# Performance work log

Hardware: AMD Instinct MI355X
Metric: run time of the kernel (lower is better)

Reference implementation:

```python
import jax, jax.numpy as jnp
import numpy as np
from jax import lax

KERNEL = 5  # cv2 np.ones((5,5)) structuring element
EDGE_WEIGHT = 0.1


def _edge_weights(target):
    # target: [B,1,H,W] float. Binary mask -> morphological gradient via
    # max-pool (dilate) and min-pool (erode) with 5x5 window, SAME padding.
    # cv2 pads dilate with -inf and erode with +inf, so padding never
    # creates or removes foreground; reduce_window init values match that.
    b = (target > 0.5).astype(target.dtype)
    win = (1, 1, KERNEL, KERNEL)
    ones = (1, 1, 1, 1)
    dilated = lax.reduce_window(b, jnp.float32(-jnp.inf), lax.max, win, ones, 'SAME')
    eroded = lax.reduce_window(b, jnp.float32(jnp.inf), lax.min, win, ones, 'SAME')
    edge = dilated - eroded
    # Samples with empty masks get edge==0 everywhere, so the per-sample
    # binary_mask.sum()>0 guard in the original is a no-op here.
    return jnp.where(edge > 0, jnp.float32(EDGE_WEIGHT), jnp.float32(1.0))


def setup_inputs() -> dict:
    key = jax.random.key(0)
    k1, k2 = jax.random.split(key)
    shape = (32, 1, 1024, 1024)
    pred = jax.random.normal(k1, shape, dtype=jnp.float32)
    target = jax.random.randint(k2, shape, 0, 2).astype(jnp.float32)
    return {"pred": pred, "target": target}


def reference(pred, target):
    # BCEWithLogitsLoss(reduction='none'): softplus(x) - x*t (stable form)
    loss = jax.nn.softplus(pred) - pred * target
    # Weighting branch only taken when target.max()==1 and target.min()==0
    cond = jnp.logical_and(target.max() == 1.0, target.min() == 0.0)
    weights = _edge_weights(target)
    weights = jnp.where(cond, weights, jnp.float32(1.0))
    return (loss * weights).mean()
```

## Files before the change

kernel.cpp:

```cpp
#include <hip/hip_runtime.h>


#define IMG     1024
#define BAND    32
#define NBANDS  (IMG / BAND)
#define NIMG    32
#define WORDS   16
#define HALO    2
#define MAXROWS (BAND + 2 * HALO)
#define NTOT    33554432.0

typedef unsigned long long u64;

__device__ __forceinline__ unsigned encf(float f) {
    unsigned u = __float_as_uint(f);
    return (u & 0x80000000u) ? ~u : (u | 0x80000000u);
}
__device__ __forceinline__ float decf(unsigned e) {
    unsigned u = (e & 0x80000000u) ? (e & 0x7fffffffu) : ~e;
    return __uint_as_float(u);
}

__global__ void bbl_init(double* dws, unsigned* uws) {
    if (threadIdx.x == 0) {
        dws[0] = 0.0; dws[1] = 0.0;
        uws[0] = 0xFFFFFFFFu;
        uws[1] = 0u;
    }
}

__global__ __launch_bounds__(512) void bbl_main(
        const float* __restrict__ pred,
        const float* __restrict__ target,
        double* __restrict__ dws, unsigned* __restrict__ uws) {
    __shared__ u64 Bm[MAXROWS][WORDS];
    __shared__ u64 Vd[BAND][WORDS];
    __shared__ u64 Ve[BAND][WORDS];
    __shared__ u64 Em[BAND][WORDS];
    __shared__ float    redS1[8], redSe[8];
    __shared__ unsigned redMn[8], redMx[8];

    const int tid  = threadIdx.x;
    const int lane = tid & 63;
    const int wid  = tid >> 6;
    const int img  = blockIdx.x / NBANDS;
    const int r0   = (blockIdx.x % NBANDS) * BAND;
    const int hs   = max(r0 - HALO, 0);
    const int he   = min(r0 + BAND + HALO, IMG);
    const int nLoaded = he - hs;
    const size_t base = (size_t)img * IMG * IMG;

    float vmin = 3.4e38f, vmax = -3.4e38f;

    for (int lr = wid; lr < nLoaded; lr += 8) {
        const float4* rowp = (const float4*)(target + base + (size_t)(hs + lr) * IMG);
        #pragma unroll
        for (int it = 0; it < 4; ++it) {
            float4 v = rowp[it * 64 + lane];
            vmin = fminf(vmin, fminf(fminf(v.x, v.y), fminf(v.z, v.w)));
            vmax = fmaxf(vmax, fmaxf(fmaxf(v.x, v.y), fmaxf(v.z, v.w)));
            u64 b0 = __ballot(v.x > 0.5f);
            u64 b1 = __ballot(v.y > 0.5f);
            u64 b2 = __ballot(v.z > 0.5f);
            u64 b3 = __ballot(v.w > 0.5f);
            if (lane < 4) {
                u64 w = (lane == 0) ? b0 : (lane == 1) ? b1 : (lane == 2) ? b2 : b3;
                Bm[lr][it * 4 + lane] = w;
            }
        }
    }
    __syncthreads();

    {
        const int orow = tid >> 4, w = tid & 15;
        const int gr = r0 + orow;
        const int lo = max(gr - 2, 0), hi = min(gr + 2, IMG - 1);
        u64 vd = 0ULL, ve = ~0ULL;
        for (int g = lo; g <= hi; ++g) { u64 b = Bm[g - hs][w]; vd |= b; ve &= b; }
        Vd[orow][w] = vd; Ve[orow][w] = ve;
    }
    __syncthreads();

    {
        const int orow = tid >> 4, w = tid & 15;
        const int k = w & 3;
        u64 hd = Vd[orow][w], he_ = Ve[orow][w];
        #pragma unroll
        for (int dd = 0; dd < 4; ++dd) {
            const int delta = (dd < 2) ? dd - 2 : dd - 1;
            const int kp = k + delta;
            u64 td, te;
            if (kp >= 0 && kp <= 3) {
                td = Vd[orow][w + delta];
                te = Ve[orow][w + delta];
            } else if (kp > 3) {
                const int wi = w + delta - 4, wn = w + delta;
                u64 nd = (wn <= 15) ? Vd[orow][wn] : 0ULL;
                u64 ne = (wn <= 15) ? Ve[orow][wn] : ~0ULL;
                td = (Vd[orow][wi] >> 1) | (nd << 63);
                te = (Ve[orow][wi] >> 1) | (ne << 63);
            } else {
                const int wi = w + delta + 4, wn = w + delta;
                u64 nd = (wn >= 0) ? Vd[orow][wn] : 0ULL;
                u64 ne = (wn >= 0) ? Ve[orow][wn] : ~0ULL;
                td = (Vd[orow][wi] << 1) | (nd >> 63);
                te = (Ve[orow][wi] << 1) | (ne >> 63);
            }
            hd |= td; he_ &= te;
        }
        Em[orow][w] = hd & ~he_;
    }
    __syncthreads();

    float s1 = 0.f, se = 0.f;
    for (int orow = wid * 4; orow < wid * 4 + 4; ++orow) {
        const int gr = r0 + orow, lr = gr - hs;
        const float4* rowp = (const float4*)(pred + base + (size_t)gr * IMG);
        #pragma unroll
        for (int it = 0; it < 4; ++it) {
            float4 p = rowp[it * 64 + lane];
            u64 e0 = Em[orow][it * 4 + 0], e1 = Em[orow][it * 4 + 1];
            u64 e2 = Em[orow][it * 4 + 2], e3 = Em[orow][it * 4 + 3];
            u64 t0 = Bm[lr][it * 4 + 0],   t1 = Bm[lr][it * 4 + 1];
            u64 t2 = Bm[lr][it * 4 + 2],   t3 = Bm[lr][it * 4 + 3];
            float x, t, loss;
            x = p.x; t = (float)((unsigned)((t0 >> lane) & 1ULL));
            loss = fmaxf(x, 0.f) - x * t + __logf(1.f + __expf(-fabsf(x)));
            s1 += loss; se += ((e0 >> lane) & 1ULL) ? loss : 0.f;
            x = p.y; t = (float)((unsigned)((t1 >> lane) & 1ULL));
            loss = fmaxf(x, 0.f) - x * t + __logf(1.f + __expf(-fabsf(x)));
            s1 += loss; se += ((e1 >> lane) & 1ULL) ? loss : 0.f;
            x = p.z; t = (float)((unsigned)((t2 >> lane) & 1ULL));
            loss = fmaxf(x, 0.f) - x * t + __logf(1.f + __expf(-fabsf(x)));
            s1 += loss; se += ((e2 >> lane) & 1ULL) ? loss : 0.f;
            x = p.w; t = (float)((unsigned)((t3 >> lane) & 1ULL));
            loss = fmaxf(x, 0.f) - x * t + __logf(1.f + __expf(-fabsf(x)));
            s1 += loss; se += ((e3 >> lane) & 1ULL) ? loss : 0.f;
        }
    }

    for (int off = 32; off > 0; off >>= 1) {
        s1   += __shfl_down(s1, off);
        se   += __shfl_down(se, off);
        vmin  = fminf(vmin, __shfl_down(vmin, off));
        vmax  = fmaxf(vmax, __shfl_down(vmax, off));
    }
    if (lane == 0) {
        redS1[wid] = s1; redSe[wid] = se;
        redMn[wid] = encf(vmin); redMx[wid] = encf(vmax);
    }
    __syncthreads();
    if (tid == 0) {
        float S1 = 0.f, Se = 0.f; unsigned mn = 0xFFFFFFFFu, mx = 0u;
        #pragma unroll
        for (int i = 0; i < 8; ++i) {
            S1 += redS1[i]; Se += redSe[i];
            mn = min(mn, redMn[i]); mx = max(mx, redMx[i]);
        }
        atomicAdd(&dws[0], (double)S1);
        atomicAdd(&dws[1], (double)Se);
        atomicMin(&uws[0], mn);
        atomicMax(&uws[1], mx);
    }
}

__global__ void bbl_fin(const double* __restrict__ dws,
                        const unsigned* __restrict__ uws,
                        float* __restrict__ out) {
    if (threadIdx.x == 0) {
        float fmin = decf(uws[0]);
        float fmax = decf(uws[1]);
        bool cond = (fmax == 1.0f) && (fmin == 0.0f);
        double s = cond ? (dws[0] - 0.9 * dws[1]) : dws[0];
        out[0] = (float)(s / NTOT);
    }
}

extern "C" void kernel_launch(void* const* d_in, const int* in_sizes, int n_in,
                              void* d_out, int out_size, void* d_ws, size_t ws_size,
                              hipStream_t stream) {
    const float* pred   = (const float*)d_in[0];
    const float* target = (const float*)d_in[1];
    double*   dws = (double*)d_ws;
    unsigned* uws = (unsigned*)(dws + 2);
    float*    out = (float*)d_out;

    hipLaunchKernelGGL(bbl_init, dim3(1), dim3(64), 0, stream, dws, uws);
    hipLaunchKernelGGL(bbl_main, dim3(NIMG * NBANDS), dim3(512), 0, stream,
                       pred, target, dws, uws);
    hipLaunchKernelGGL(bbl_fin, dim3(1), dim3(64), 0, stream, dws, uws, out);
}
```

Before: 296.3 us.

## Split target bit-packing into separate pass to avoid halo re-reads

Adds a first kernel that reads the target once, packs it into per-row 64-bit masks in workspace and computes min/max. A second kernel loads only the packed bits, including halo rows, plus pred to compute the loss. This removes the halo re-reads of the float target and lightens the main kernel. In exchange it adds a global write and read of the packed mask, an extra launch and a serialization point between the kernels. It also pads shared arrays and issues the pred loads up front. The old fused kernel is kept as a fallback when the workspace is too small.

```diff
diff --git a/kernel.cpp b/kernel.cpp
--- a/kernel.cpp
+++ b/kernel.cpp
@@ -6,8 +6,10 @@
 #define NBANDS  (IMG / BAND)
 #define NIMG    32
 #define WORDS   16
+#define WPAD    17
 #define HALO    2
 #define MAXROWS (BAND + 2 * HALO)
+#define NROWS   (NIMG * IMG)
 #define NTOT    33554432.0
 
 typedef unsigned long long u64;
@@ -29,16 +31,74 @@
     }
 }
 
-__global__ __launch_bounds__(512) void bbl_main(
+__global__ __launch_bounds__(256) void bbl_bits(
+        const float* __restrict__ target,
+        u64* __restrict__ bits, unsigned* __restrict__ uws) {
+    __shared__ unsigned redMn[4], redMx[4];
+    const int tid  = threadIdx.x;
+    const int lane = tid & 63;
+    const int wv   = tid >> 6;
+    const int waveId = blockIdx.x * 4 + wv;
+    const int nWaves = gridDim.x * 4;
+
+    float vmin = 3.4e38f, vmax = -3.4e38f;
+
+    for (int row = waveId; row < NROWS; row += nWaves) {
+        const float4* rowp = (const float4*)(target + (size_t)row * IMG);
+        float4 v0 = rowp[lane];
+        float4 v1 = rowp[64 + lane];
+        float4 v2 = rowp[128 + lane];
+        float4 v3 = rowp[192 + lane];
+
+        vmin = fminf(vmin, fminf(fminf(v0.x, v0.y), fminf(v0.z, v0.w)));
+        vmax = fmaxf(vmax, fmaxf(fmaxf(v0.x, v0.y), fmaxf(v0.z, v0.w)));
+        vmin = fminf(vmin, fminf(fminf(v1.x, v1.y), fminf(v1.z, v1.w)));
+        vmax = fmaxf(vmax, fmaxf(fmaxf(v1.x, v1.y), fmaxf(v1.z, v1.w)));
+        vmin = fminf(vmin, fminf(fminf(v2.x, v2.y), fminf(v2.z, v2.w)));
+        vmax = fmaxf(vmax, fmaxf(fmaxf(v2.x, v2.y), fmaxf(v2.z, v2.w)));
+        vmin = fminf(vmin, fminf(fminf(v3.x, v3.y), fminf(v3.z, v3.w)));
+        vmax = fmaxf(vmax, fmaxf(fmaxf(v3.x, v3.y), fmaxf(v3.z, v3.w)));
+
+        u64 myw = 0ULL;
+        #pragma unroll
+        for (int it = 0; it < 4; ++it) {
+            float4 v = (it == 0) ? v0 : (it == 1) ? v1 : (it == 2) ? v2 : v3;
+            u64 b0 = __ballot(v.x > 0.5f);
+            u64 b1 = __ballot(v.y > 0.5f);
+            u64 b2 = __ballot(v.z > 0.5f);
+            u64 b3 = __ballot(v.w > 0.5f);
+            if ((lane >> 2) == it) {
+                const int m = lane & 3;
+                myw = (m == 0) ? b0 : (m == 1) ? b1 : (m == 2) ? b2 : b3;
+            }
+        }
+        if (lane < 16) bits[(size_t)row * WORDS + lane] = myw;
+    }
+
+    for (int off = 32; off > 0; off >>= 1) {
+        vmin = fminf(vmin, __shfl_down(vmin, off));
+        vmax = fmaxf(vmax, __shfl_down(vmax, off));
+    }
+    if (lane == 0) { redMn[wv] = encf(vmin); redMx[wv] = encf(vmax); }
+    __syncthreads();
+    if (tid == 0) {
+        unsigned mn = 0xFFFFFFFFu, mx = 0u;
+        #pragma unroll
+        for (int i = 0; i < 4; ++i) { mn = min(mn, redMn[i]); mx = max(mx, redMx[i]); }
+        atomicMin(&uws[0], mn);
+        atomicMax(&uws[1], mx);
+    }
+}
+
+__global__ __launch_bounds__(512) void bbl_loss(
         const float* __restrict__ pred,
-        const float* __restrict__ target,
-        double* __restrict__ dws, unsigned* __restrict__ uws) {
-    __shared__ u64 Bm[MAXROWS][WORDS];
-    __shared__ u64 Vd[BAND][WORDS];
-    __shared__ u64 Ve[BAND][WORDS];
-    __shared__ u64 Em[BAND][WORDS];
-    __shared__ float    redS1[8], redSe[8];
-    __shared__ unsigned redMn[8], redMx[8];
+        const u64* __restrict__ bits,
+        double* __restrict__ dws) {
+    __shared__ u64 Bm[MAXROWS][WPAD];
+    __shared__ u64 Vd[BAND][WPAD];
+    __shared__ u64 Ve[BAND][WPAD];
+    __shared__ u64 Em[BAND][WPAD];
+    __shared__ float redS1[8], redSe[8];
 
     const int tid  = threadIdx.x;
     const int lane = tid & 63;
@@ -50,24 +110,10 @@
     const int nLoaded = he - hs;
     const size_t base = (size_t)img * IMG * IMG;
 
-    float vmin = 3.4e38f, vmax = -3.4e38f;
-
-    for (int lr = wid; lr < nLoaded; lr += 8) {
-        const float4* rowp = (const float4*)(target + base + (size_t)(hs + lr) * IMG);
-        #pragma unroll
-        for (int it = 0; it < 4; ++it) {
-            float4 v = rowp[it * 64 + lane];
-            vmin = fminf(vmin, fminf(fminf(v.x, v.y), fminf(v.z, v.w)));
-            vmax = fmaxf(vmax, fmaxf(fmaxf(v.x, v.y), fmaxf(v.z, v.w)));
-            u64 b0 = __ballot(v.x > 0.5f);
-            u64 b1 = __ballot(v.y > 0.5f);
-            u64 b2 = __ballot(v.z > 0.5f);
-            u64 b3 = __ballot(v.w > 0.5f);
-            if (lane < 4) {
-                u64 w = (lane == 0) ? b0 : (lane == 1) ? b1 : (lane == 2) ? b2 : b3;
-                Bm[lr][it * 4 + lane] = w;
-            }
-        }
+    {
+        const u64* gb = bits + ((size_t)img * IMG + hs) * WORDS;
+        for (int i = tid; i < nLoaded * WORDS; i += 512)
+            Bm[i >> 4][i & 15] = gb[i];
     }
     __syncthreads();
 
@@ -116,6 +162,137 @@
     for (int orow = wid * 4; orow < wid * 4 + 4; ++orow) {
         const int gr = r0 + orow, lr = gr - hs;
         const float4* rowp = (const float4*)(pred + base + (size_t)gr * IMG);
+        float4 p0 = rowp[lane];
+        float4 p1 = rowp[64 + lane];
+        float4 p2 = rowp[128 + lane];
+        float4 p3 = rowp[192 + lane];
+        #pragma unroll
+        for (int it = 0; it < 4; ++it) {
+            float4 p = (it == 0) ? p0 : (it == 1) ? p1 : (it == 2) ? p2 : p3;
+            u64 e0 = Em[orow][it * 4 + 0], e1 = Em[orow][it * 4 + 1];
+            u64 e2 = Em[orow][it * 4 + 2], e3 = Em[orow][it * 4 + 3];
+            u64 t0 = Bm[lr][it * 4 + 0],   t1 = Bm[lr][it * 4 + 1];
+            u64 t2 = Bm[lr][it * 4 + 2],   t3 = Bm[lr][it * 4 + 3];
+            float x, l;
+            x = p.x;
+            l = fmaxf(x, 0.f) + __logf(1.f + __expf(-fabsf(x)))
+                - (((t0 >> lane) & 1ULL) ? x : 0.f);
+            s1 += l; se += ((e0 >> lane) & 1ULL) ? l : 0.f;
+            x = p.y;
+            l = fmaxf(x, 0.f) + __logf(1.f + __expf(-fabsf(x)))
+                - (((t1 >> lane) & 1ULL) ? x : 0.f);
+            s1 += l; se += ((e1 >> lane) & 1ULL) ? l : 0.f;
+            x = p.z;
+            l = fmaxf(x, 0.f) + __logf(1.f + __expf(-fabsf(x)))
+                - (((t2 >> lane) & 1ULL) ? x : 0.f);
+            s1 += l; se += ((e2 >> lane) & 1ULL) ? l : 0.f;
+            x = p.w;
+            l = fmaxf(x, 0.f) + __logf(1.f + __expf(-fabsf(x)))
+                - (((t3 >> lane) & 1ULL) ? x : 0.f);
+            s1 += l; se += ((e3 >> lane) & 1ULL) ? l : 0.f;
+        }
+    }
+
+    for (int off = 32; off > 0; off >>= 1) {
+        s1 += __shfl_down(s1, off);
+        se += __shfl_down(se, off);
+    }
+    if (lane == 0) { redS1[wid] = s1; redSe[wid] = se; }
+    __syncthreads();
+    if (tid == 0) {
+        float S1 = 0.f, Se = 0.f;
+        #pragma unroll
+        for (int i = 0; i < 8; ++i) { S1 += redS1[i]; Se += redSe[i]; }
+        atomicAdd(&dws[0], (double)S1);
+        atomicAdd(&dws[1], (double)Se);
+    }
+}
+
+__global__ __launch_bounds__(512) void bbl_main(
+        const float* __restrict__ pred,
+        const float* __restrict__ target,
+        double* __restrict__ dws, unsigned* __restrict__ uws) {
+    __shared__ u64 Bm[MAXROWS][WORDS];
+    __shared__ u64 Vd[BAND][WORDS];
+    __shared__ u64 Ve[BAND][WORDS];
+    __shared__ u64 Em[BAND][WORDS];
+    __shared__ float    redS1[8], redSe[8];
+    __shared__ unsigned redMn[8], redMx[8];
+
+    const int tid  = threadIdx.x;
+    const int lane = tid & 63;
+    const int wid  = tid >> 6;
+    const int img  = blockIdx.x / NBANDS;
+    const int r0   = (blockIdx.x % NBANDS) * BAND;
+    const int hs   = max(r0 - HALO, 0);
+    const int he   = min(r0 + BAND + HALO, IMG);
+    const int nLoaded = he - hs;
+    const size_t base = (size_t)img * IMG * IMG;
+
+    float vmin = 3.4e38f, vmax = -3.4e38f;
+
+    for (int lr = wid; lr < nLoaded; lr += 8) {
+        const float4* rowp = (const float4*)(target + base + (size_t)(hs + lr) * IMG);
+        #pragma unroll
+        for (int it = 0; it < 4; ++it) {
+            float4 v = rowp[it * 64 + lane];
+            vmin = fminf(vmin, fminf(fminf(v.x, v.y), fminf(v.z, v.w)));
+            vmax = fmaxf(vmax, fmaxf(fmaxf(v.x, v.y), fmaxf(v.z, v.w)));
+            u64 b0 = __ballot(v.x > 0.5f);
+            u64 b1 = __ballot(v.y > 0.5f);
+            u64 b2 = __ballot(v.z > 0.5f);
+            u64 b3 = __ballot(v.w > 0.5f);
+            if (lane < 4) {
+                u64 w = (lane == 0) ? b0 : (lane == 1) ? b1 : (lane == 2) ? b2 : b3;
+                Bm[lr][it * 4 + lane] = w;
+            }
+        }
+    }
+    __syncthreads();
+    {
+        const int orow = tid >> 4, w = tid & 15;
+        const int gr = r0 + orow;
+        const int lo = max(gr - 2, 0), hi = min(gr + 2, IMG - 1);
+        u64 vd = 0ULL, ve = ~0ULL;
+        for (int g = lo; g <= hi; ++g) { u64 b = Bm[g - hs][w]; vd |= b; ve &= b; }
+        Vd[orow][w] = vd; Ve[orow][w] = ve;
+    }
+    __syncthreads();
+    {
+        const int orow = tid >> 4, w = tid & 15;
+        const int k = w & 3;
+        u64 hd = Vd[orow][w], he_ = Ve[orow][w];
+        #pragma unroll
+        for (int dd = 0; dd < 4; ++dd) {
+            const int delta = (dd < 2) ? dd - 2 : dd - 1;
+            const int kp = k + delta;
+            u64 td, te;
+            if (kp >= 0 && kp <= 3) {
+                td = Vd[orow][w + delta];
+                te = Ve[orow][w + delta];
+            } else if (kp > 3) {
+                const int wi = w + delta - 4, wn = w + delta;
+                u64 nd = (wn <= 15) ? Vd[orow][wn] : 0ULL;
+                u64 ne = (wn <= 15) ? Ve[orow][wn] : ~0ULL;
+                td = (Vd[orow][wi] >> 1) | (nd << 63);
+                te = (Ve[orow][wi] >> 1) | (ne << 63);
+            } else {
+                const int wi = w + delta + 4, wn = w + delta;
+                u64 nd = (wn >= 0) ? Vd[orow][wn] : 0ULL;
+                u64 ne = (wn >= 0) ? Ve[orow][wn] : ~0ULL;
+                td = (Vd[orow][wi] << 1) | (nd >> 63);
+                te = (Ve[orow][wi] << 1) | (ne >> 63);
+            }
+            hd |= td; he_ &= te;
+        }
+        Em[orow][w] = hd & ~he_;
+    }
+    __syncthreads();
+
+    float s1 = 0.f, se = 0.f;
+    for (int orow = wid * 4; orow < wid * 4 + 4; ++orow) {
+        const int gr = r0 + orow, lr = gr - hs;
+        const float4* rowp = (const float4*)(pred + base + (size_t)gr * IMG);
         #pragma unroll
         for (int it = 0; it < 4; ++it) {
             float4 p = rowp[it * 64 + lane];
@@ -185,8 +362,19 @@
     unsigned* uws = (unsigned*)(dws + 2);
     float*    out = (float*)d_out;
 
+    const size_t bits_off   = 64;
+    const size_t bits_bytes = (size_t)NROWS * WORDS * sizeof(u64);
+
     hipLaunchKernelGGL(bbl_init, dim3(1), dim3(64), 0, stream, dws, uws);
-    hipLaunchKernelGGL(bbl_main, dim3(NIMG * NBANDS), dim3(512), 0, stream,
-                       pred, target, dws, uws);
+    if (ws_size >= bits_off + bits_bytes) {
+        u64* bits = (u64*)((char*)d_ws + bits_off);
+        hipLaunchKernelGGL(bbl_bits, dim3(2048), dim3(256), 0, stream,
+                           target, bits, uws);
+        hipLaunchKernelGGL(bbl_loss, dim3(NIMG * NBANDS), dim3(512), 0, stream,
+                           pred, bits, dws);
+    } else {
+        hipLaunchKernelGGL(bbl_main, dim3(NIMG * NBANDS), dim3(512), 0, stream,
+                           pred, target, dws, uws);
+    }
     hipLaunchKernelGGL(bbl_fin, dim3(1), dim3(64), 0, stream, dws, uws, out);
 }
```

After: 308.1 us. +4.0%, slower.

## Split fused kernel into bit-pack, edge, and loss passes via workspace planes

Applied to the files above, without the earlier changes.

Replaces the single banded kernel with three kernels: one packs the target into a global bitmask plane while also reducing min/max, one computes the 5x5 morphological edge plane using wave shuffles instead of shared memory, and one streams pred with the bit planes to accumulate the loss sums. The aim is to drop the redundant halo reads of target and the shared-memory syncs, and to give each pass a simple grid-stride streaming pattern with two loads in flight. In exchange it adds two extra launches and the write and read of 8 MB of bit planes, and it falls back to the old kernel when the workspace is too small.

```diff
diff --git a/kernel.cpp b/kernel.cpp
--- a/kernel.cpp
+++ b/kernel.cpp
@@ -8,6 +8,9 @@
 #define WORDS   16
 #define HALO    2
 #define MAXROWS (BAND + 2 * HALO)
+#define NROWS   (NIMG * IMG)
+#define NGRP    (NROWS * 4)
+#define NWAVES  8192
 #define NTOT    33554432.0
 
 typedef unsigned long long u64;
@@ -26,6 +29,177 @@
         dws[0] = 0.0; dws[1] = 0.0;
         uws[0] = 0xFFFFFFFFu;
         uws[1] = 0u;
+    }
+}
+
+__global__ __launch_bounds__(256) void bbl_bits(
+        const float* __restrict__ target,
+        u64* __restrict__ bits, unsigned* __restrict__ uws) {
+    __shared__ unsigned redMn[4], redMx[4];
+    const int tid  = threadIdx.x;
+    const int lane = tid & 63;
+    const int wv   = tid >> 6;
+    const int waveId = __builtin_amdgcn_readfirstlane(blockIdx.x * 4 + wv);
+
+    float vmin = 3.4e38f, vmax = -3.4e38f;
+    const float4* tp = (const float4*)target;
+
+    for (int g = waveId; g < NGRP; g += 2 * NWAVES) {
+        const int g2 = g + NWAVES;
+        float4 a = tp[(size_t)g  * 64 + lane];
+        float4 b = tp[(size_t)g2 * 64 + lane];
+
+        vmin = fminf(vmin, fminf(fminf(a.x, a.y), fminf(a.z, a.w)));
+        vmax = fmaxf(vmax, fmaxf(fmaxf(a.x, a.y), fmaxf(a.z, a.w)));
+        vmin = fminf(vmin, fminf(fminf(b.x, b.y), fminf(b.z, b.w)));
+        vmax = fmaxf(vmax, fmaxf(fmaxf(b.x, b.y), fmaxf(b.z, b.w)));
+
+        u64 a0 = __ballot(a.x > 0.5f), a1 = __ballot(a.y > 0.5f);
+        u64 a2 = __ballot(a.z > 0.5f), a3 = __ballot(a.w > 0.5f);
+        u64 b0 = __ballot(b.x > 0.5f), b1 = __ballot(b.y > 0.5f);
+        u64 b2 = __ballot(b.z > 0.5f), b3 = __ballot(b.w > 0.5f);
+
+        const int m = lane & 3;
+        u64 wa = (m == 0) ? a0 : (m == 1) ? a1 : (m == 2) ? a2 : a3;
+        u64 wb = (m == 0) ? b0 : (m == 1) ? b1 : (m == 2) ? b2 : b3;
+        if (lane < 8) {
+            const int gg = (lane < 4) ? g : g2;
+            bits[(size_t)gg * 4 + m] = (lane < 4) ? wa : wb;
+        }
+    }
+
+    for (int off = 32; off > 0; off >>= 1) {
+        vmin = fminf(vmin, __shfl_down(vmin, off));
+        vmax = fmaxf(vmax, __shfl_down(vmax, off));
+    }
+    if (lane == 0) { redMn[wv] = encf(vmin); redMx[wv] = encf(vmax); }
+    __syncthreads();
+    if (tid == 0) {
+        unsigned mn = 0xFFFFFFFFu, mx = 0u;
+        #pragma unroll
+        for (int i = 0; i < 4; ++i) { mn = min(mn, redMn[i]); mx = max(mx, redMx[i]); }
+        atomicMin(&uws[0], mn);
+        atomicMax(&uws[1], mx);
+    }
+}
+
+__global__ __launch_bounds__(256) void bbl_edge(
+        const u64* __restrict__ bits, u64* __restrict__ eplane) {
+    const int tid  = threadIdx.x;
+    const int lane = tid & 63;
+    const int wv   = tid >> 6;
+    const int waveId = __builtin_amdgcn_readfirstlane(blockIdx.x * 4 + wv);
+
+    const int R  = waveId * 4 + (lane >> 4);
+    const int r  = R & (IMG - 1);
+    const int rb = R - r;
+    const int w  = lane & 15;
+
+    const int lo = max(r - 2, 0), hi = min(r + 2, IMG - 1);
+    u64 vd = 0ULL, ve = ~0ULL;
+    for (int rr = lo; rr <= hi; ++rr) {
+        u64 b = bits[(size_t)(rb + rr) * WORDS + w];
+        vd |= b; ve &= b;
+    }
+
+    const int k = w & 3;
+    u64 hd = vd, he_ = ve;
+    #pragma unroll
+    for (int dd = 0; dd < 4; ++dd) {
+        const int delta = (dd < 2) ? dd - 2 : dd - 1;
+        const int kp = k + delta;
+        u64 td, te;
+        if (kp >= 0 && kp <= 3) {
+            td = __shfl(vd, w + delta, 16);
+            te = __shfl(ve, w + delta, 16);
+        } else if (kp > 3) {
+            const int wi = w + delta - 4, wn = w + delta;
+            u64 vdi = __shfl(vd, wi, 16),      vei = __shfl(ve, wi, 16);
+            u64 vdn = __shfl(vd, wn & 15, 16), ven = __shfl(ve, wn & 15, 16);
+            u64 nd = (wn <= 15) ? vdn : 0ULL;
+            u64 ne = (wn <= 15) ? ven : ~0ULL;
+            td = (vdi >> 1) | (nd << 63);
+            te = (vei >> 1) | (ne << 63);
+        } else {
+            const int wi = w + delta + 4, wn = w + delta;
+            u64 vdi = __shfl(vd, wi, 16),      vei = __shfl(ve, wi, 16);
+            u64 vdn = __shfl(vd, wn & 15, 16), ven = __shfl(ve, wn & 15, 16);
+            u64 nd = (wn >= 0) ? vdn : 0ULL;
+            u64 ne = (wn >= 0) ? ven : ~0ULL;
+            td = (vdi << 1) | (nd >> 63);
+            te = (vei << 1) | (ne >> 63);
+        }
+        hd |= td; he_ &= te;
+    }
+    eplane[(size_t)R * WORDS + w] = hd & ~he_;
+}
+
+__global__ __launch_bounds__(256) void bbl_loss(
+        const float* __restrict__ pred,
+        const u64* __restrict__ bits, const u64* __restrict__ eplane,
+        double* __restrict__ dws) {
+    __shared__ float redS1[4], redSe[4];
+    const int tid  = threadIdx.x;
+    const int lane = tid & 63;
+    const int wv   = tid >> 6;
+    const int waveId = __builtin_amdgcn_readfirstlane(blockIdx.x * 4 + wv);
+
+    float s1 = 0.f, se = 0.f;
+    const float4* pp = (const float4*)pred;
+
+    for (int g = waveId; g < NGRP; g += 2 * NWAVES) {
+        const int g2 = g + NWAVES;
+        float4 a = pp[(size_t)g  * 64 + lane];
+        float4 b = pp[(size_t)g2 * 64 + lane];
+        u64 ta0 = bits[(size_t)g * 4 + 0],   ta1 = bits[(size_t)g * 4 + 1];
+        u64 ta2 = bits[(size_t)g * 4 + 2],   ta3 = bits[(size_t)g * 4 + 3];
+        u64 ea0 = eplane[(size_t)g * 4 + 0], ea1 = eplane[(size_t)g * 4 + 1];
+        u64 ea2 = eplane[(size_t)g * 4 + 2], ea3 = eplane[(size_t)g * 4 + 3];
+        u64 tb0 = bits[(size_t)g2 * 4 + 0],   tb1 = bits[(size_t)g2 * 4 + 1];
+        u64 tb2 = bits[(size_t)g2 * 4 + 2],   tb3 = bits[(size_t)g2 * 4 + 3];
+        u64 eb0 = eplane[(size_t)g2 * 4 + 0], eb1 = eplane[(size_t)g2 * 4 + 1];
+        u64 eb2 = eplane[(size_t)g2 * 4 + 2], eb3 = eplane[(size_t)g2 * 4 + 3];
+
+        float x, l;
+        x = a.x; l = fmaxf(x, 0.f) + __logf(1.f + __expf(-fabsf(x)))
+                    - (((ta0 >> lane) & 1ULL) ? x : 0.f);
+        s1 += l; se += ((ea0 >> lane) & 1ULL) ? l : 0.f;
+        x = a.y; l = fmaxf(x, 0.f) + __logf(1.f + __expf(-fabsf(x)))
+                    - (((ta1 >> lane) & 1ULL) ? x : 0.f);
+        s1 += l; se += ((ea1 >> lane) & 1ULL) ? l : 0.f;
+        x = a.z; l = fmaxf(x, 0.f) + __logf(1.f + __expf(-fabsf(x)))
+                    - (((ta2 >> lane) & 1ULL) ? x : 0.f);
+        s1 += l; se += ((ea2 >> lane) & 1ULL) ? l : 0.f;
+        x = a.w; l = fmaxf(x, 0.f) + __logf(1.f + __expf(-fabsf(x)))
+                    - (((ta3 >> lane) & 1ULL) ? x : 0.f);
+        s1 += l; se += ((ea3 >> lane) & 1ULL) ? l : 0.f;
+
+        x = b.x; l = fmaxf(x, 0.f) + __logf(1.f + __expf(-fabsf(x)))
+                    - (((tb0 >> lane) & 1ULL) ? x : 0.f);
+        s1 += l; se += ((eb0 >> lane) & 1ULL) ? l : 0.f;
+        x = b.y; l = fmaxf(x, 0.f) + __logf(1.f + __expf(-fabsf(x)))
+                    - (((tb1 >> lane) & 1ULL) ? x : 0.f);
+        s1 += l; se += ((eb1 >> lane) & 1ULL) ? l : 0.f;
+        x = b.z; l = fmaxf(x, 0.f) + __logf(1.f + __expf(-fabsf(x)))
+                    - (((tb2 >> lane) & 1ULL) ? x : 0.f);
+        s1 += l; se += ((eb2 >> lane) & 1ULL) ? l : 0.f;
+        x = b.w; l = fmaxf(x, 0.f) + __logf(1.f + __expf(-fabsf(x)))
+                    - (((tb3 >> lane) & 1ULL) ? x : 0.f);
+        s1 += l; se += ((eb3 >> lane) & 1ULL) ? l : 0.f;
+    }
+
+    for (int off = 32; off > 0; off >>= 1) {
+        s1 += __shfl_down(s1, off);
+        se += __shfl_down(se, off);
+    }
+    if (lane == 0) { redS1[wv] = s1; redSe[wv] = se; }
+    __syncthreads();
+    if (tid == 0) {
+        float S1 = 0.f, Se = 0.f;
+        #pragma unroll
+        for (int i = 0; i < 4; ++i) { S1 += redS1[i]; Se += redSe[i]; }
+        atomicAdd(&dws[0], (double)S1);
+        atomicAdd(&dws[1], (double)Se);
     }
 }
 
@@ -70,7 +244,6 @@
         }
     }
     __syncthreads();
-
     {
         const int orow = tid >> 4, w = tid & 15;
         const int gr = r0 + orow;
@@ -80,7 +253,6 @@
         Vd[orow][w] = vd; Ve[orow][w] = ve;
     }
     __syncthreads();
-
     {
         const int orow = tid >> 4, w = tid & 15;
         const int k = w & 3;
@@ -185,8 +357,23 @@
     unsigned* uws = (unsigned*)(dws + 2);
     float*    out = (float*)d_out;
 
+    const size_t bits_off  = 64;
+    const size_t plane_sz  = (size_t)NROWS * WORDS * sizeof(u64);
+    const size_t need      = bits_off + 2 * plane_sz;
+
     hipLaunchKernelGGL(bbl_init, dim3(1), dim3(64), 0, stream, dws, uws);
-    hipLaunchKernelGGL(bbl_main, dim3(NIMG * NBANDS), dim3(512), 0, stream,
-                       pred, target, dws, uws);
+    if (ws_size >= need) {
+        u64* bits   = (u64*)((char*)d_ws + bits_off);
+        u64* eplane = bits + (size_t)NROWS * WORDS;
+        hipLaunchKernelGGL(bbl_bits, dim3(2048), dim3(256), 0, stream,
+                           target, bits, uws);
+        hipLaunchKernelGGL(bbl_edge, dim3(2048), dim3(256), 0, stream,
+                           bits, eplane);
+        hipLaunchKernelGGL(bbl_loss, dim3(2048), dim3(256), 0, stream,
+                           pred, bits, eplane, dws);
+    } else {
+        hipLaunchKernelGGL(bbl_main, dim3(NIMG * NBANDS), dim3(512), 0, stream,
+                           pred, target, dws, uws);
+    }
     hipLaunchKernelGGL(bbl_fin, dim3(1), dim3(64), 0, stream, dws, uws, out);
 }
```

Measured after the change: 356.4 us. 1.2x slower.

## Halve block size and have each thread load two rows ahead of use

Applied to the files above, without the earlier changes.

The block shrinks from 512 to 256 threads, and every stage is reworked so each wave or thread covers twice as many rows. In the load stage, the target rows lr and lr+4, and the pred row pairs, are all fetched into registers up front before any compute. The goal is more memory loads in flight per wave to hide global-memory latency in what looks like a latency-bound kernel. The cost is higher register pressure, which could lower occupancy, and fewer threads per block doing the shared-memory bit-mask stages.

```diff
diff --git a/kernel.cpp b/kernel.cpp
--- a/kernel.cpp
+++ b/kernel.cpp
@@ -29,7 +29,7 @@
     }
 }
 
-__global__ __launch_bounds__(512) void bbl_main(
+__global__ __launch_bounds__(256) void bbl_main(
         const float* __restrict__ pred,
         const float* __restrict__ target,
         double* __restrict__ dws, unsigned* __restrict__ uws) {
@@ -37,8 +37,8 @@
     __shared__ u64 Vd[BAND][WORDS];
     __shared__ u64 Ve[BAND][WORDS];
     __shared__ u64 Em[BAND][WORDS];
-    __shared__ float    redS1[8], redSe[8];
-    __shared__ unsigned redMn[8], redMx[8];
+    __shared__ float    redS1[4], redSe[4];
+    __shared__ unsigned redMn[4], redMx[4];
 
     const int tid  = threadIdx.x;
     const int lane = tid & 63;
@@ -49,80 +49,153 @@
     const int he   = min(r0 + BAND + HALO, IMG);
     const int nLoaded = he - hs;
     const size_t base = (size_t)img * IMG * IMG;
+    const float* tb = target + base;
 
     float vmin = 3.4e38f, vmax = -3.4e38f;
 
+    #pragma unroll 1
     for (int lr = wid; lr < nLoaded; lr += 8) {
-        const float4* rowp = (const float4*)(target + base + (size_t)(hs + lr) * IMG);
+        const int lrB = lr + 4;
+        const bool hb = (lrB < nLoaded);
+        const float* rA = tb + (size_t)(hs + lr) * IMG + 4 * lane;
+        float4 a0 = *(const float4*)(rA);
+        float4 a1 = *(const float4*)(rA + 256);
+        float4 a2 = *(const float4*)(rA + 512);
+        float4 a3 = *(const float4*)(rA + 768);
+        float4 d0, d1, d2, d3;
+        if (hb) {
+            const float* rB = tb + (size_t)(hs + lrB) * IMG + 4 * lane;
+            d0 = *(const float4*)(rB);
+            d1 = *(const float4*)(rB + 256);
+            d2 = *(const float4*)(rB + 512);
+            d3 = *(const float4*)(rB + 768);
+        }
         #pragma unroll
         for (int it = 0; it < 4; ++it) {
-            float4 v = rowp[it * 64 + lane];
+            float4 v = (it == 0) ? a0 : (it == 1) ? a1 : (it == 2) ? a2 : a3;
             vmin = fminf(vmin, fminf(fminf(v.x, v.y), fminf(v.z, v.w)));
             vmax = fmaxf(vmax, fmaxf(fmaxf(v.x, v.y), fmaxf(v.z, v.w)));
-            u64 b0 = __ballot(v.x > 0.5f);
-            u64 b1 = __ballot(v.y > 0.5f);
-            u64 b2 = __ballot(v.z > 0.5f);
-            u64 b3 = __ballot(v.w > 0.5f);
+            u64 c0 = __ballot(v.x > 0.5f);
+            u64 c1 = __ballot(v.y > 0.5f);
+            u64 c2 = __ballot(v.z > 0.5f);
+            u64 c3 = __ballot(v.w > 0.5f);
             if (lane < 4) {
-                u64 w = (lane == 0) ? b0 : (lane == 1) ? b1 : (lane == 2) ? b2 : b3;
+                u64 w = (lane == 0) ? c0 : (lane == 1) ? c1 : (lane == 2) ? c2 : c3;
                 Bm[lr][it * 4 + lane] = w;
             }
         }
+        if (hb) {
+            #pragma unroll
+            for (int it = 0; it < 4; ++it) {
+                float4 v = (it == 0) ? d0 : (it == 1) ? d1 : (it == 2) ? d2 : d3;
+                vmin = fminf(vmin, fminf(fminf(v.x, v.y), fminf(v.z, v.w)));
+                vmax = fmaxf(vmax, fmaxf(fmaxf(v.x, v.y), fmaxf(v.z, v.w)));
+                u64 c0 = __ballot(v.x > 0.5f);
+                u64 c1 = __ballot(v.y > 0.5f);
+                u64 c2 = __ballot(v.z > 0.5f);
+                u64 c3 = __ballot(v.w > 0.5f);
+                if (lane < 4) {
+                    u64 w = (lane == 0) ? c0 : (lane == 1) ? c1 : (lane == 2) ? c2 : c3;
+                    Bm[lrB][it * 4 + lane] = w;
+                }
+            }
+        }
     }
     __syncthreads();
 
     {
-        const int orow = tid >> 4, w = tid & 15;
-        const int gr = r0 + orow;
-        const int lo = max(gr - 2, 0), hi = min(gr + 2, IMG - 1);
-        u64 vd = 0ULL, ve = ~0ULL;
-        for (int g = lo; g <= hi; ++g) { u64 b = Bm[g - hs][w]; vd |= b; ve &= b; }
-        Vd[orow][w] = vd; Ve[orow][w] = ve;
+        const int w = tid & 15;
+        #pragma unroll
+        for (int half = 0; half < 2; ++half) {
+            const int orow = (tid >> 4) + half * 16;
+            const int gr = r0 + orow;
+            const int lo = max(gr - 2, 0), hi = min(gr + 2, IMG - 1);
+            u64 vd = 0ULL, ve = ~0ULL;
+            for (int g = lo; g <= hi; ++g) { u64 bb = Bm[g - hs][w]; vd |= bb; ve &= bb; }
+            Vd[orow][w] = vd; Ve[orow][w] = ve;
+        }
     }
     __syncthreads();
 
     {
-        const int orow = tid >> 4, w = tid & 15;
+        const int w = tid & 15;
         const int k = w & 3;
-        u64 hd = Vd[orow][w], he_ = Ve[orow][w];
-        #pragma unroll
-        for (int dd = 0; dd < 4; ++dd) {
-            const int delta = (dd < 2) ? dd - 2 : dd - 1;
-            const int kp = k + delta;
-            u64 td, te;
-            if (kp >= 0 && kp <= 3) {
-                td = Vd[orow][w + delta];
-                te = Ve[orow][w + delta];
-            } else if (kp > 3) {
-                const int wi = w + delta - 4, wn = w + delta;
-                u64 nd = (wn <= 15) ? Vd[orow][wn] : 0ULL;
-                u64 ne = (wn <= 15) ? Ve[orow][wn] : ~0ULL;
-                td = (Vd[orow][wi] >> 1) | (nd << 63);
-                te = (Ve[orow][wi] >> 1) | (ne << 63);
-            } else {
-                const int wi = w + delta + 4, wn = w + delta;
-                u64 nd = (wn >= 0) ? Vd[orow][wn] : 0ULL;
-                u64 ne = (wn >= 0) ? Ve[orow][wn] : ~0ULL;
-                td = (Vd[orow][wi] << 1) | (nd >> 63);
-                te = (Ve[orow][wi] << 1) | (ne >> 63);
+        #pragma unroll
+        for (int half = 0; half < 2; ++half) {
+            const int orow = (tid >> 4) + half * 16;
+            u64 hd = Vd[orow][w], he_ = Ve[orow][w];
+            #pragma unroll
+            for (int dd = 0; dd < 4; ++dd) {
+                const int delta = (dd < 2) ? dd - 2 : dd - 1;
+                const int kp = k + delta;
+                u64 td, te;
+                if (kp >= 0 && kp <= 3) {
+                    td = Vd[orow][w + delta];
+                    te = Ve[orow][w + delta];
+                } else if (kp > 3) {
+                    const int wi = w + delta - 4, wn = w + delta;
+                    u64 nd = (wn <= 15) ? Vd[orow][wn] : 0ULL;
+                    u64 ne = (wn <= 15) ? Ve[orow][wn] : ~0ULL;
+                    td = (Vd[orow][wi] >> 1) | (nd << 63);
+                    te = (Ve[orow][wi] >> 1) | (ne << 63);
+                } else {
+                    const int wi = w + delta + 4, wn = w + delta;
+                    u64 nd = (wn >= 0) ? Vd[orow][wn] : 0ULL;
+                    u64 ne = (wn >= 0) ? Ve[orow][wn] : ~0ULL;
+                    td = (Vd[orow][wi] << 1) | (nd >> 63);
+                    te = (Ve[orow][wi] << 1) | (ne >> 63);
+                }
+                hd |= td; he_ &= te;
             }
-            hd |= td; he_ &= te;
-        }
-        Em[orow][w] = hd & ~he_;
+            Em[orow][w] = hd & ~he_;
+        }
     }
     __syncthreads();
 
     float s1 = 0.f, se = 0.f;
-    for (int orow = wid * 4; orow < wid * 4 + 4; ++orow) {
-        const int gr = r0 + orow, lr = gr - hs;
-        const float4* rowp = (const float4*)(pred + base + (size_t)gr * IMG);
+    const float* pb = pred + base;
+    #pragma unroll 1
+    for (int jp = 0; jp < 8; jp += 2) {
+        const int oA = wid * 8 + jp, oB = oA + 1;
+        const int lrA = r0 + oA - hs, lrB = r0 + oB - hs;
+        const float* rA = pb + (size_t)(r0 + oA) * IMG + 4 * lane;
+        const float* rB = pb + (size_t)(r0 + oB) * IMG + 4 * lane;
+        float4 pA0 = *(const float4*)(rA);
+        float4 pA1 = *(const float4*)(rA + 256);
+        float4 pA2 = *(const float4*)(rA + 512);
+        float4 pA3 = *(const float4*)(rA + 768);
+        float4 pB0 = *(const float4*)(rB);
+        float4 pB1 = *(const float4*)(rB + 256);
+        float4 pB2 = *(const float4*)(rB + 512);
+        float4 pB3 = *(const float4*)(rB + 768);
         #pragma unroll
         for (int it = 0; it < 4; ++it) {
-            float4 p = rowp[it * 64 + lane];
-            u64 e0 = Em[orow][it * 4 + 0], e1 = Em[orow][it * 4 + 1];
-            u64 e2 = Em[orow][it * 4 + 2], e3 = Em[orow][it * 4 + 3];
-            u64 t0 = Bm[lr][it * 4 + 0],   t1 = Bm[lr][it * 4 + 1];
-            u64 t2 = Bm[lr][it * 4 + 2],   t3 = Bm[lr][it * 4 + 3];
+            float4 p = (it == 0) ? pA0 : (it == 1) ? pA1 : (it == 2) ? pA2 : pA3;
+            u64 e0 = Em[oA][it * 4 + 0], e1 = Em[oA][it * 4 + 1];
+            u64 e2 = Em[oA][it * 4 + 2], e3 = Em[oA][it * 4 + 3];
+            u64 t0 = Bm[lrA][it * 4 + 0], t1 = Bm[lrA][it * 4 + 1];
+            u64 t2 = Bm[lrA][it * 4 + 2], t3 = Bm[lrA][it * 4 + 3];
+            float x, t, loss;
+            x = p.x; t = (float)((unsigned)((t0 >> lane) & 1ULL));
+            loss = fmaxf(x, 0.f) - x * t + __logf(1.f + __expf(-fabsf(x)));
+            s1 += loss; se += ((e0 >> lane) & 1ULL) ? loss : 0.f;
+            x = p.y; t = (float)((unsigned)((t1 >> lane) & 1ULL));
+            loss = fmaxf(x, 0.f) - x * t + __logf(1.f + __expf(-fabsf(x)));
+            s1 += loss; se += ((e1 >> lane) & 1ULL) ? loss : 0.f;
+            x = p.z; t = (float)((unsigned)((t2 >> lane) & 1ULL));
+            loss = fmaxf(x, 0.f) - x * t + __logf(1.f + __expf(-fabsf(x)));
+            s1 += loss; se += ((e2 >> lane) & 1ULL) ? loss : 0.f;
+            x = p.w; t = (float)((unsigned)((t3 >> lane) & 1ULL));
+            loss = fmaxf(x, 0.f) - x * t + __logf(1.f + __expf(-fabsf(x)));
+            s1 += loss; se += ((e3 >> lane) & 1ULL) ? loss : 0.f;
+        }
+        #pragma unroll
+        for (int it = 0; it < 4; ++it) {
+            float4 p = (it == 0) ? pB0 : (it == 1) ? pB1 : (it == 2) ? pB2 : pB3;
+            u64 e0 = Em[oB][it * 4 + 0], e1 = Em[oB][it * 4 + 1];
+            u64 e2 = Em[oB][it * 4 + 2], e3 = Em[oB][it * 4 + 3];
+            u64 t0 = Bm[lrB][it * 4 + 0], t1 = Bm[lrB][it * 4 + 1];
+            u64 t2 = Bm[lrB][it * 4 + 2], t3 = Bm[lrB][it * 4 + 3];
             float x, t, loss;
             x = p.x; t = (float)((unsigned)((t0 >> lane) & 1ULL));
             loss = fmaxf(x, 0.f) - x * t + __logf(1.f + __expf(-fabsf(x)));
@@ -153,7 +226,7 @@
     if (tid == 0) {
         float S1 = 0.f, Se = 0.f; unsigned mn = 0xFFFFFFFFu, mx = 0u;
         #pragma unroll
-        for (int i = 0; i < 8; ++i) {
+        for (int i = 0; i < 4; ++i) {
             S1 += redS1[i]; Se += redSe[i];
             mn = min(mn, redMn[i]); mx = max(mx, redMx[i]);
         }
@@ -186,7 +259,7 @@
     float*    out = (float*)d_out;
 
     hipLaunchKernelGGL(bbl_init, dim3(1), dim3(64), 0, stream, dws, uws);
-    hipLaunchKernelGGL(bbl_main, dim3(NIMG * NBANDS), dim3(512), 0, stream,
+    hipLaunchKernelGGL(bbl_main, dim3(NIMG * NBANDS), dim3(256), 0, stream,
                        pred, target, dws, uws);
     hipLaunchKernelGGL(bbl_fin, dim3(1), dim3(64), 0, stream, dws, uws, out);
 }
```

Result: no change. 297.7 us (+0.5%).
